# Kernel optimization log

Measured on AMD Instinct MI355X. Metric: run time of the kernel, lower is better.

The kernel has to match this reference:

```python
import jax, jax.numpy as jnp
import numpy as np

L, H, R, N, E = 6, 128, 64, 10000, 160000
SSILU_SCALE = 1.0 / 0.6  # ScaledSiLU
INV_SQRT_3 = 1.0 / np.sqrt(3.0)
INV_SQRT_H = 1.0 / np.sqrt(H)
INV_SQRT_2 = 1.0 / np.sqrt(2.0)


def ssilu(x):
    return jax.nn.silu(x) * SSILU_SCALE


def lnorm(x, w, b):
    m = x.mean(-1, keepdims=True)
    v = jnp.var(x, axis=-1, keepdims=True)
    return (x - m) * jax.lax.rsqrt(v + 1e-5) * w + b


def gated_block(x, v, wv1, wv2, wu1, bu1, wu2, bu2, hout):
    # GatedEquivariantBlock: x [N,Hin], v [N,3,Hin]
    vec1 = jnp.linalg.norm(jnp.einsum('nci,io->nco', v, wv1), axis=-2)  # [N,Hin]
    vec2 = jnp.einsum('nci,io->nco', v, wv2)                            # [N,3,hout]
    h = ssilu(jnp.concatenate([x, vec1], -1) @ wu1 + bu1) @ wu2 + bu2   # [N,2*hout]
    xs, xv = h[..., :hout], h[..., hout:]
    return ssilu(xs), xv[:, None, :] * vec2


def forward_impl(edge_index, x, vec, edge_rbf, edge_vector,
                 ln_w, ln_b, xp1_w, xp1_b, xp2_w, xp2_b, rbf_w, rbf_b,
                 vp_w, xv1_w, xv1_b, xv2_w, xv2_b,
                 we1, be1, we2, be2,
                 g1_v1, g1_v2, g1_u1, g1_u1b, g1_u2, g1_u2b,
                 g2_v1, g2_v2, g2_u1, g2_u1b, g2_u2, g2_u2b):
    src, dst = edge_index[0], edge_index[1]  # message flows src(j) -> dst(i)
    for l in range(L):
        # ---- PaiNNMessage ----
        xh = ssilu(lnorm(x, ln_w[l], ln_b[l]) @ xp1_w[l] + xp1_b[l]) @ xp2_w[l] + xp2_b[l]  # [N,3H]
        rbfh = edge_rbf @ rbf_w[l] + rbf_b[l]                                                # [E,3H]
        m = xh[src] * rbfh                                                                    # gather + elementwise
        mx = m[:, :H]
        m2 = m[:, H:2 * H] * INV_SQRT_3
        m3 = m[:, 2 * H:]
        mvec = (vec[src] * m2[:, None, :] + m3[:, None, :] * edge_vector[:, :, None]) * INV_SQRT_H  # [E,3,H]
        dx = jax.ops.segment_sum(mx, dst, num_segments=N)
        dvec = jax.ops.segment_sum(mvec, dst, num_segments=N)
        x = (x + dx) * INV_SQRT_2
        vec = vec + dvec
        # ---- PaiNNUpdate ----
        vp = jnp.einsum('nci,io->nco', vec, vp_w[l])  # [N,3,2H]
        v1, v2 = vp[..., :H], vp[..., H:]
        vec_dot = (v1 * v2).sum(axis=1) * INV_SQRT_H  # [N,H]
        vnorm = jnp.sqrt((v2 ** 2).sum(axis=-2) + 1e-8)
        h = ssilu(jnp.concatenate([x, vnorm], -1) @ xv1_w[l] + xv1_b[l]) @ xv2_w[l] + xv2_b[l]  # [N,3H]
        xu1, xu2, xu3 = h[:, :H], h[:, H:2 * H], h[:, 2 * H:]
        x = x + (xu1 + xu2 * vec_dot) * INV_SQRT_2
        vec = vec + xu3[:, None, :] * v1
        # ScaleFactor is identity without a scale file
    energy = ssilu(x @ we1 + be1) @ we2 + be2  # [N,1] per-atom energy
    fx, fv = gated_block(x, vec, g1_v1, g1_v2, g1_u1, g1_u1b, g1_u2, g1_u2b, H // 2)
    fx, fv = gated_block(fx, fv, g2_v1, g2_v2, g2_u1, g2_u1b, g2_u2, g2_u2b, 1)
    forces = fv[..., 0]  # [N,3]
    return jnp.concatenate([energy, forces], axis=-1)  # [N,4] packed (energy, fx, fy, fz)


def setup_inputs() -> dict:
    key = jax.random.key(0)
    ks = iter(jax.random.split(key, 64))
    nrm = lambda shape, s=0.05: jax.random.normal(next(ks), shape, jnp.float32) * s
    return dict(
        x=jax.random.normal(next(ks), (N, H), jnp.float32),
        vec=jax.random.normal(next(ks), (N, 3, H), jnp.float32),
        edge_index=jax.random.randint(next(ks), (2, E), 0, N),
        edge_rbf=jax.random.uniform(next(ks), (E, R), jnp.float32),
        edge_vector=jax.random.normal(next(ks), (E, 3), jnp.float32),
        ln_w=jnp.ones((L, H)), ln_b=jnp.zeros((L, H)),
        xp1_w=nrm((L, H, H)), xp1_b=jnp.zeros((L, H)),
        xp2_w=nrm((L, H, 3 * H)), xp2_b=jnp.zeros((L, 3 * H)),
        rbf_w=nrm((L, R, 3 * H)), rbf_b=jnp.zeros((L, 3 * H)),
        vp_w=nrm((L, H, 2 * H)),
        xv1_w=nrm((L, 2 * H, H)), xv1_b=jnp.zeros((L, H)),
        xv2_w=nrm((L, H, 3 * H)), xv2_b=jnp.zeros((L, 3 * H)),
        we1=nrm((H, H // 2)), be1=jnp.zeros((H // 2,)),
        we2=nrm((H // 2, 1)), be2=jnp.zeros((1,)),
        g1_v1=nrm((H, H)), g1_v2=nrm((H, H // 2)),
        g1_u1=nrm((2 * H, H)), g1_u1b=jnp.zeros((H,)),
        g1_u2=nrm((H, H)), g1_u2b=jnp.zeros((H,)),
        g2_v1=nrm((H // 2, H // 2)), g2_v2=nrm((H // 2, 1)),
        g2_u1=nrm((H, H // 2)), g2_u1b=jnp.zeros((H // 2,)),
        g2_u2=nrm((H // 2, 2)), g2_u2b=jnp.zeros((2,)),
    )


def reference(x, vec, edge_index, edge_rbf, edge_vector,
              ln_w, ln_b, xp1_w, xp1_b, xp2_w, xp2_b, rbf_w, rbf_b,
              vp_w, xv1_w, xv1_b, xv2_w, xv2_b,
              we1, be1, we2, be2,
              g1_v1, g1_v2, g1_u1, g1_u1b, g1_u2, g1_u2b,
              g2_v1, g2_v2, g2_u1, g2_u1b, g2_u2, g2_u2b):
    return forward_impl(edge_index, x, vec, edge_rbf, edge_vector,
                        ln_w, ln_b, xp1_w, xp1_b, xp2_w, xp2_b, rbf_w, rbf_b,
                        vp_w, xv1_w, xv1_b, xv2_w, xv2_b,
                        we1, be1, we2, be2,
                        g1_v1, g1_v2, g1_u1, g1_u1b, g1_u2, g1_u2b,
                        g2_v1, g2_v2, g2_u1, g2_u1b, g2_u2, g2_u2b)
```

## Files before the change

kernel.cpp:

```cpp
#include <hip/hip_runtime.h>
#include <hip/hip_bf16.h>

#define NN 10000
#define EE 160000
#define LL 6

#define INV_SQRT_3f  0.57735026919f
#define INV_SQRT_Hf  0.08838834764832f
#define INV_SQRT_2f  0.70710678118655f

typedef _Float16 half8 __attribute__((ext_vector_type(8)));
typedef float f32x4 __attribute__((ext_vector_type(4)));

#define WE1OFF   0
#define WV1OFF   8192
#define WV2OFF   24576
#define WU1OFF   32768
#define WU2OFF   65536
#define G2V1OFF  81920
#define G2U1OFF  86016
#define WFIN_SZ  94208

__device__ __forceinline__ float ssilu_f(float v){
  float s = 1.0f / (1.0f + __expf(-v));
  return v * s * 1.6666666666667f;
}

__global__ __launch_bounds__(256) void k_hist(const int* __restrict__ edst, int* __restrict__ cnt){
  int i = blockIdx.x*256 + threadIdx.x;
  if (i < EE) atomicAdd(&cnt[edst[i]], 1);
}

__global__ __launch_bounds__(1024) void k_scan(const int* __restrict__ cnt,
                                               int* __restrict__ off, int* __restrict__ cur){
  __shared__ int ps[1024];
  int t = threadIdx.x;
  int base = t*10;
  int local[10];
  int s = 0;
  #pragma unroll
  for (int i=0;i<10;i++){
    int c = (base+i < NN) ? cnt[base+i] : 0;
    local[i] = s; s += c;
  }
  ps[t] = s;
  __syncthreads();
  for (int d=1; d<1024; d<<=1){
    int v = (t>=d) ? ps[t-d] : 0;
    __syncthreads();
    ps[t] += v;
    __syncthreads();
  }
  int pre = (t>0) ? ps[t-1] : 0;
  #pragma unroll
  for (int i=0;i<10;i++){
    int idx = base+i;
    if (idx < NN){ int o = pre + local[i]; off[idx]=o; cur[idx]=o; }
  }
  if (t==1023) off[NN] = ps[1023];
}

__global__ __launch_bounds__(256) void k_fill(const int* __restrict__ edst,
                                              int* __restrict__ cur, int* __restrict__ eord){
  int i = blockIdx.x*256 + threadIdx.x;
  if (i < EE){
    int d = edst[i];
    int p = atomicAdd(&cur[d], 1);
    eord[p] = i;
  }
}

__global__ __launch_bounds__(256) void k_sorta(const float* __restrict__ erbf,
                                               const int* __restrict__ eord, _Float16* __restrict__ eA){
  long i = (long)blockIdx.x*256 + threadIdx.x;
  if (i >= (long)EE*64) return;
  int j = i & 7, lane = (i >> 3) & 63, kh = (i >> 9) & 1;
  long tile = i >> 10;
  int e = eord[tile*16 + (lane&15)];
  eA[i] = (_Float16)erbf[(size_t)e*64 + kh*32 + (lane>>4)*8 + j];
}

__global__ __launch_bounds__(256) void k_sorte(const int* __restrict__ esrc, const float* __restrict__ evec,
                                               const int* __restrict__ eord, float4* __restrict__ es4){
  int p = blockIdx.x*256 + threadIdx.x;
  if (p >= EE) return;
  int e = eord[p];
  es4[p] = make_float4(evec[(size_t)e*3], evec[(size_t)e*3+1], evec[(size_t)e*3+2],
                       __int_as_float(esrc[e]));
}

__global__ __launch_bounds__(256) void k_packw(const float* __restrict__ w, _Float16* __restrict__ wf){
  int i = blockIdx.x*256 + threadIdx.x;
  if (i >= LL*24*2*64*8) return;
  int j    = i & 7;
  int lane = (i >> 3) & 63;
  int kh   = (i >> 9) & 1;
  int rest = i >> 10;
  int nb   = rest % 24;
  int l    = rest / 24;
  int k    = 32*kh + 8*(lane>>4) + j;
  int ch   = nb*16 + (lane&15);
  float v = w[((size_t)l*64 + k)*384 + ch];
  if (ch >= 128 && ch < 256) v *= INV_SQRT_3f;
  wf[i] = (_Float16)v;
}

__global__ __launch_bounds__(256) void k_packb(const float* __restrict__ b, float* __restrict__ bsc){
  int i = blockIdx.x*256 + threadIdx.x;
  if (i >= LL*384) return;
  int ch = i % 384;
  float v = b[i];
  if (ch >= 128 && ch < 256) v *= INV_SQRT_3f;
  bsc[i] = v;
}

struct PackTab {
  const float* s[40];
  _Float16* d[40];
  int K[40];
  int NO[40];
};
__global__ __launch_bounds__(256) void k_packall(PackTab tb){
  int e = blockIdx.y;
  int K = tb.K[e], NO = tb.NO[e];
  int tot = K*NO, KS = K >> 5;
  const float* s = tb.s[e];
  _Float16* d = tb.d[e];
  for (int i = blockIdx.x*256 + threadIdx.x; i < tot; i += gridDim.x*256){
    int j = i & 7, lane = (i >> 3) & 63, rest = i >> 9;
    int ks = rest % KS, nb = rest / KS;
    int k = ks*32 + (lane>>4)*8 + j, n = nb*16 + (lane&15);
    d[i] = (_Float16)s[(size_t)k*NO + n];
  }
}

__global__ __launch_bounds__(256) void k_cvt16v(const float* __restrict__ v, _Float16* __restrict__ xv){
  int i = blockIdx.x*256 + threadIdx.x;
  if (i >= NN*384) return;
  int node = i / 384, r = i % 384;
  xv[(size_t)node*768 + 384 + r] = (_Float16)v[i];
}

__global__ __launch_bounds__(256) void k_xhgemm(
    const float* __restrict__ x,
    const float* __restrict__ lnw, const float* __restrict__ lnb,
    const _Float16* __restrict__ wf1, const float* __restrict__ b1,
    const _Float16* __restrict__ wf2, const float* __restrict__ b2,
    _Float16* __restrict__ xv16,
    const _Float16* __restrict__ eA, const _Float16* __restrict__ wf,
    const float* __restrict__ bsc, _Float16* __restrict__ rbfh)
{
  __shared__ _Float16 sA[32][136];
  __shared__ _Float16 sH[32][136];
  int t = threadIdx.x;
  if (blockIdx.x >= 313){
    int ob = (blockIdx.x - 313)*4 + (t >> 6);
    int lane = t & 63;
    int i0 = ob * 64;
    int tg = ob * 4;
    int ml = lane & 15, kg = lane >> 4;
    half8 a0[4], a1[4];
    #pragma unroll
    for (int tt = 0; tt < 4; tt++){
      a0[tt] = *(const half8*)(eA + ((size_t)((tg+tt)*2+0)*64 + lane)*8);
      a1[tt] = *(const half8*)(eA + ((size_t)((tg+tt)*2+1)*64 + lane)*8);
    }
    #pragma unroll 2
    for (int nb = 0; nb < 24; nb++){
      half8 b0 = *(const half8*)(wf + ((size_t)(nb*2+0)*64 + lane)*8);
      half8 b1h = *(const half8*)(wf + ((size_t)(nb*2+1)*64 + lane)*8);
      float bias = bsc[nb*16 + ml];
      #pragma unroll
      for (int tt = 0; tt < 4; tt++){
        f32x4 acc = {bias, bias, bias, bias};
        acc = __builtin_amdgcn_mfma_f32_16x16x32_f16(a0[tt], b0, acc, 0, 0, 0);
        acc = __builtin_amdgcn_mfma_f32_16x16x32_f16(a1[tt], b1h, acc, 0, 0, 0);
        _Float16* orow = rbfh + (size_t)(i0 + tt*16)*384 + nb*16 + ml;
        #pragma unroll
        for (int r = 0; r < 4; r++)
          orow[(size_t)(kg*4 + r)*384] = (_Float16)acc[r];
      }
    }
    return;
  }
  int n0 = blockIdx.x * 32;
  {
    int nd = t >> 3, sb = t & 7;
    int node = n0 + nd;
    float v[16];
    float s = 0.f, ss = 0.f;
    if (node < NN){
      const float* xr = x + (size_t)node*128 + sb*16;
      #pragma unroll
      for (int g = 0; g < 4; g++){
        float4 q = *(const float4*)(xr + g*4);
        v[g*4+0]=q.x; v[g*4+1]=q.y; v[g*4+2]=q.z; v[g*4+3]=q.w;
      }
      #pragma unroll
      for (int u = 0; u < 16; u++){ s += v[u]; ss += v[u]*v[u]; }
    } else {
      #pragma unroll
      for (int u = 0; u < 16; u++) v[u] = 0.f;
    }
    #pragma unroll
    for (int o2 = 4; o2 > 0; o2 >>= 1){
      s  += __shfl_xor(s, o2, 8);
      ss += __shfl_xor(ss, o2, 8);
    }
    float mean = s * (1.0f/128.0f);
    float var  = ss * (1.0f/128.0f) - mean*mean;
    float rstd = rsqrtf(var + 1e-5f);
    #pragma unroll
    for (int u = 0; u < 16; u++){
      int h = sb*16 + u;
      sA[nd][h] = (node < NN) ? (_Float16)((v[u]-mean)*rstd*lnw[h] + lnb[h]) : (_Float16)0.f;
    }
  }
  __syncthreads();
  int lane = t & 63, w = t >> 6, ml = lane & 15, kg = lane >> 4;
  int mt = w >> 1;
  {
    half8 a[4];
    #pragma unroll
    for (int ks = 0; ks < 4; ks++)
      a[ks] = *(const half8*)&sA[mt*16 + ml][ks*32 + kg*8];
    float hout[4][4];
    #pragma unroll
    for (int nb4 = 0; nb4 < 4; nb4++){
      int nb = (w&1)*4 + nb4;
      float bias = b1[nb*16 + ml];
      f32x4 acc = {bias, bias, bias, bias};
      #pragma unroll
      for (int ks = 0; ks < 4; ks++)
        acc = __builtin_amdgcn_mfma_f32_16x16x32_f16(a[ks],
                *(const half8*)(wf1 + ((size_t)(nb*4+ks)*64 + lane)*8), acc, 0,0,0);
      #pragma unroll
      for (int r = 0; r < 4; r++) hout[nb4][r] = ssilu_f(acc[r]);
    }
    #pragma unroll
    for (int nb4 = 0; nb4 < 4; nb4++){
      int nb = (w&1)*4 + nb4;
      #pragma unroll
      for (int r = 0; r < 4; r++)
        sH[mt*16 + kg*4 + r][nb*16 + ml] = (_Float16)hout[nb4][r];
    }
  }
  __syncthreads();
  {
    half8 a[4];
    #pragma unroll
    for (int ks = 0; ks < 4; ks++)
      a[ks] = *(const half8*)&sH[mt*16 + ml][ks*32 + kg*8];
    #pragma unroll 4
    for (int nb12 = 0; nb12 < 12; nb12++){
      int nb = (w&1)*12 + nb12;
      float bias = b2[nb*16 + ml];
      f32x4 acc = {bias, bias, bias, bias};
      #pragma unroll
      for (int ks = 0; ks < 4; ks++)
        acc = __builtin_amdgcn_mfma_f32_16x16x32_f16(a[ks],
                *(const half8*)(wf2 + ((size_t)(nb*4+ks)*64 + lane)*8), acc, 0,0,0);
      #pragma unroll
      for (int r = 0; r < 4; r++){
        int m = mt*16 + kg*4 + r;
        int node = n0 + m;
        if (node < NN) xv16[(size_t)node*768 + nb*16 + ml] = (_Float16)acc[r];
      }
    }
  }
}

__global__ __launch_bounds__(256) void k_edge3(
    const _Float16* __restrict__ rbfh,
    const float4* __restrict__ es4, const int* __restrict__ off,
    const _Float16* __restrict__ xv16,
    _Float16* __restrict__ dx, _Float16* __restrict__ dvec)
{
  int t = threadIdx.x;
  int lane = t & 63;
  int n = blockIdx.x*4 + (t>>6);
  if (n >= NN) return;
  int o0 = off[n], o1 = off[n+1];
  float ax0 = 0.f, ax1 = 0.f;
  float av00=0.f, av01=0.f, av10=0.f, av11=0.f, av20=0.f, av21=0.f;
  #pragma unroll 2
  for (int p = o0; p < o1; p++){
    const _Float16* hr = rbfh + (size_t)p*384;
    float h0 = (float)hr[lane];
    float h1 = (float)hr[64+lane];
    float h2 = (float)hr[128+lane];
    float h3 = (float)hr[192+lane];
    float h4 = (float)hr[256+lane];
    float h5 = (float)hr[320+lane];
    float4 q = es4[p];
    int sN = __float_as_int(q.w);
    const _Float16* xr = xv16 + (size_t)sN*768;
    float m0  = h0 * (float)xr[lane];
    float m1  = h1 * (float)xr[64+lane];
    float m2a = h2 * (float)xr[128+lane];
    float m2b = h3 * (float)xr[192+lane];
    float m3a = h4 * (float)xr[256+lane];
    float m3b = h5 * (float)xr[320+lane];
    ax0 += m0; ax1 += m1;
    const _Float16* vr = xr + 384;
    av00 = fmaf((float)vr[lane],     m2a, av00); av00 = fmaf(m3a, q.x, av00);
    av01 = fmaf((float)vr[64+lane],  m2b, av01); av01 = fmaf(m3b, q.x, av01);
    av10 = fmaf((float)vr[128+lane], m2a, av10); av10 = fmaf(m3a, q.y, av10);
    av11 = fmaf((float)vr[192+lane], m2b, av11); av11 = fmaf(m3b, q.y, av11);
    av20 = fmaf((float)vr[256+lane], m2a, av20); av20 = fmaf(m3a, q.z, av20);
    av21 = fmaf((float)vr[320+lane], m2b, av21); av21 = fmaf(m3b, q.z, av21);
  }
  _Float16* dxr = dx + (size_t)n*128;
  dxr[lane] = (_Float16)ax0; dxr[64+lane] = (_Float16)ax1;
  _Float16* dvr = dvec + (size_t)n*384;
  dvr[lane]     = (_Float16)(av00 * INV_SQRT_Hf);
  dvr[64+lane]  = (_Float16)(av01 * INV_SQRT_Hf);
  dvr[128+lane] = (_Float16)(av10 * INV_SQRT_Hf);
  dvr[192+lane] = (_Float16)(av11 * INV_SQRT_Hf);
  dvr[256+lane] = (_Float16)(av20 * INV_SQRT_Hf);
  dvr[320+lane] = (_Float16)(av21 * INV_SQRT_Hf);
}

__global__ __launch_bounds__(256) void k_node_mfma(
    float* __restrict__ xbuf, float* __restrict__ vbuf,
    const _Float16* __restrict__ dx, const _Float16* __restrict__ dvec,
    const _Float16* __restrict__ wfvp,
    const _Float16* __restrict__ wfxv1, const float* __restrict__ xv1_b,
    const _Float16* __restrict__ wfxv2, const float* __restrict__ xv2_b,
    _Float16* __restrict__ xv16)
{
  __shared__ _Float16 sCat[32][264];
  int t = threadIdx.x;
  int n0 = blockIdx.x * 32;
  int lane = t & 63, w = t >> 6, ml = lane & 15, kg = lane >> 4;
  int mt = w & 1, nbb = (w >> 1) * 4;
  float v1g[3][4][4];
  float vdg[4][4];
  float vn[4][4];
  #pragma unroll
  for (int i=0;i<4;i++){
    #pragma unroll
    for (int r=0;r<4;r++){ vdg[i][r]=0.f; vn[i][r]=0.f; }
  }
  int arow = n0 + mt*16 + ml;
  bool aok = arow < NN;
  #pragma unroll
  for (int cd = 0; cd < 3; cd++){
    half8 a[4];
    #pragma unroll
    for (int ks = 0; ks < 4; ks++){
      if (aok){
        const float* vr = vbuf + (size_t)arow*384 + cd*128 + ks*32 + kg*8;
        const _Float16* dr = dvec + (size_t)arow*384 + cd*128 + ks*32 + kg*8;
        float4 q0 = *(const float4*)(vr);
        float4 q1 = *(const float4*)(vr+4);
        half8 dh = *(const half8*)(dr);
        a[ks][0]=(_Float16)(q0.x+(float)dh[0]); a[ks][1]=(_Float16)(q0.y+(float)dh[1]);
        a[ks][2]=(_Float16)(q0.z+(float)dh[2]); a[ks][3]=(_Float16)(q0.w+(float)dh[3]);
        a[ks][4]=(_Float16)(q1.x+(float)dh[4]); a[ks][5]=(_Float16)(q1.y+(float)dh[5]);
        a[ks][6]=(_Float16)(q1.z+(float)dh[6]); a[ks][7]=(_Float16)(q1.w+(float)dh[7]);
      } else {
        #pragma unroll
        for (int j=0;j<8;j++) a[ks][j] = (_Float16)0.f;
      }
    }
    #pragma unroll
    for (int nb4 = 0; nb4 < 4; nb4++){
      int nb1 = nbb + nb4;
      f32x4 acc1 = {0.f,0.f,0.f,0.f}, acc2 = {0.f,0.f,0.f,0.f};
      #pragma unroll
      for (int ks = 0; ks < 4; ks++){
        acc1 = __builtin_amdgcn_mfma_f32_16x16x32_f16(a[ks],
                 *(const half8*)(wfvp + ((size_t)(nb1*4+ks)*64 + lane)*8), acc1, 0,0,0);
        acc2 = __builtin_amdgcn_mfma_f32_16x16x32_f16(a[ks],
                 *(const half8*)(wfvp + ((size_t)((nb1+8)*4+ks)*64 + lane)*8), acc2, 0,0,0);
      }
      #pragma unroll
      for (int r = 0; r < 4; r++){
        float v1v = acc1[r], v2v = acc2[r];
        vdg[nb4][r] += v1v*v2v;
        vn[nb4][r] += v2v*v2v;
        v1g[cd][nb4][r] = v1v;
      }
    }
  }
  #pragma unroll
  for (int nb4 = 0; nb4 < 4; nb4++){
    #pragma unroll
    for (int r = 0; r < 4; r++){
      int m = mt*16 + kg*4 + r, c = (nbb+nb4)*16 + ml;
      vdg[nb4][r] *= INV_SQRT_Hf;
      sCat[m][128 + c] = (_Float16)sqrtf(vn[nb4][r] + 1e-8f);
    }
  }
  {
    int nd = t >> 3, sb = t & 7;
    int node = n0 + nd;
    if (node < NN){
      const float* xr = xbuf + (size_t)node*128 + sb*16;
      const _Float16* dr = dx + (size_t)node*128 + sb*16;
      half8 da = *(const half8*)(dr);
      half8 db = *(const half8*)(dr+8);
      #pragma unroll
      for (int g = 0; g < 4; g++){
        float4 qa = *(const float4*)(xr + g*4);
        float d0 = (float)((g<2)?da[g*4+0]:db[(g-2)*4+0]);
        float d1 = (float)((g<2)?da[g*4+1]:db[(g-2)*4+1]);
        float d2 = (float)((g<2)?da[g*4+2]:db[(g-2)*4+2]);
        float d3 = (float)((g<2)?da[g*4+3]:db[(g-2)*4+3]);
        sCat[nd][sb*16+g*4+0] = (_Float16)((qa.x+d0)*INV_SQRT_2f);
        sCat[nd][sb*16+g*4+1] = (_Float16)((qa.y+d1)*INV_SQRT_2f);
        sCat[nd][sb*16+g*4+2] = (_Float16)((qa.z+d2)*INV_SQRT_2f);
        sCat[nd][sb*16+g*4+3] = (_Float16)((qa.w+d3)*INV_SQRT_2f);
      }
    } else {
      #pragma unroll
      for (int u = 0; u < 16; u++) sCat[nd][sb*16+u] = (_Float16)0.f;
    }
  }
  __syncthreads();
  float hreg[4][4];
  {
    half8 a[8];
    #pragma unroll
    for (int ks = 0; ks < 8; ks++)
      a[ks] = *(const half8*)&sCat[mt*16 + ml][ks*32 + kg*8];
    #pragma unroll
    for (int nb4 = 0; nb4 < 4; nb4++){
      int nb = (w>>1)*4 + nb4;
      float bias = xv1_b[nb*16 + ml];
      f32x4 acc = {bias, bias, bias, bias};
      #pragma unroll
      for (int ks = 0; ks < 8; ks++)
        acc = __builtin_amdgcn_mfma_f32_16x16x32_f16(a[ks],
                *(const half8*)(wfxv1 + ((size_t)(nb*8+ks)*64 + lane)*8), acc, 0,0,0);
      #pragma unroll
      for (int r = 0; r < 4; r++) hreg[nb4][r] = ssilu_f(acc[r]);
    }
  }
  __syncthreads();
  #pragma unroll
  for (int nb4 = 0; nb4 < 4; nb4++){
    int nb = (w>>1)*4 + nb4;
    #pragma unroll
    for (int r = 0; r < 4; r++)
      sCat[mt*16 + kg*4 + r][nb*16 + ml] = (_Float16)hreg[nb4][r];
  }
  __syncthreads();
  {
    half8 a[4];
    #pragma unroll
    for (int ks = 0; ks < 4; ks++)
      a[ks] = *(const half8*)&sCat[mt*16 + ml][ks*32 + kg*8];
    #pragma unroll 2
    for (int nb4 = 0; nb4 < 4; nb4++){
      int nbu = nbb + nb4;
      float b1v = xv2_b[nbu*16 + ml];
      float b2v = xv2_b[(nbu+8)*16 + ml];
      float b3v = xv2_b[(nbu+16)*16 + ml];
      f32x4 au1 = {b1v,b1v,b1v,b1v};
      f32x4 au2 = {b2v,b2v,b2v,b2v};
      f32x4 au3 = {b3v,b3v,b3v,b3v};
      #pragma unroll
      for (int ks = 0; ks < 4; ks++){
        au1 = __builtin_amdgcn_mfma_f32_16x16x32_f16(a[ks],
                *(const half8*)(wfxv2 + ((size_t)(nbu*4+ks)*64 + lane)*8), au1, 0,0,0);
        au2 = __builtin_amdgcn_mfma_f32_16x16x32_f16(a[ks],
                *(const half8*)(wfxv2 + ((size_t)((nbu+8)*4+ks)*64 + lane)*8), au2, 0,0,0);
        au3 = __builtin_amdgcn_mfma_f32_16x16x32_f16(a[ks],
                *(const half8*)(wfxv2 + ((size_t)((nbu+16)*4+ks)*64 + lane)*8), au3, 0,0,0);
      }
      #pragma unroll
      for (int r = 0; r < 4; r++){
        int m = mt*16 + kg*4 + r;
        int node = n0 + m;
        if (node >= NN) continue;
        int c = nbu*16 + ml;
        float xu1 = au1[r], xu2 = au2[r], xu3 = au3[r];
        float vdv = vdg[nb4][r];
        size_t px = (size_t)node*128 + c;
        float xn = (xbuf[px] + (float)dx[px]) * INV_SQRT_2f;
        xbuf[px] = xn + (xu1 + xu2*vdv) * INV_SQRT_2f;
        #pragma unroll
        for (int cd = 0; cd < 3; cd++){
          float v1v = v1g[cd][nb4][r];
          size_t pv = (size_t)node*384 + cd*128 + c;
          float vo = vbuf[pv] + (float)dvec[pv] + xu3*v1v;
          vbuf[pv] = vo;
          xv16[(size_t)node*768 + 384 + cd*128 + c] = (_Float16)vo;
        }
      }
    }
  }
}

__global__ __launch_bounds__(256) void k_final(
    const float* __restrict__ x, const float* __restrict__ vec,
    const _Float16* __restrict__ wfin,
    const float* __restrict__ be1, const float* __restrict__ we2, const float* __restrict__ be2,
    const float* __restrict__ u1b, const float* __restrict__ u2b,
    const float* __restrict__ g2v2, const float* __restrict__ g2u1b, const float* __restrict__ g2u2,
    const float* __restrict__ g2u2b,
    float* __restrict__ out)
{
  __shared__ _Float16 sCat[32][264];
  __shared__ _Float16 sV2[3][32][72];
  __shared__ _Float16 sH[32][136];
  __shared__ _Float16 sFV[3][32][72];
  __shared__ _Float16 sE1[32][72];
  __shared__ float sR[3][32];
  int t = threadIdx.x;
  int n0 = blockIdx.x * 32;
  int lane = t & 63, w = t >> 6, ml = lane & 15, kg = lane >> 4;
  int mt = w & 1, nh = w >> 1;

  {
    int nd = t >> 3, sb = t & 7;
    int node = n0 + nd;
    if (node < NN){
      const float* xr = x + (size_t)node*128 + sb*16;
      #pragma unroll
      for (int g = 0; g < 4; g++){
        float4 q = *(const float4*)(xr + g*4);
        sCat[nd][sb*16+g*4+0]=(_Float16)q.x; sCat[nd][sb*16+g*4+1]=(_Float16)q.y;
        sCat[nd][sb*16+g*4+2]=(_Float16)q.z; sCat[nd][sb*16+g*4+3]=(_Float16)q.w;
      }
    } else {
      #pragma unroll
      for (int u = 0; u < 16; u++) sCat[nd][sb*16+u] = (_Float16)0.f;
    }
  }
  {
    int arow = n0 + mt*16 + ml;
    bool aok = arow < NN;
    float n1sq[4][4];
    #pragma unroll
    for (int i=0;i<4;i++){
      #pragma unroll
      for (int r=0;r<4;r++) n1sq[i][r]=0.f;
    }
    for (int cd = 0; cd < 3; cd++){
      half8 a[4];
      #pragma unroll
      for (int ks = 0; ks < 4; ks++){
        if (aok){
          const float* vr = vec + (size_t)arow*384 + cd*128 + ks*32 + kg*8;
          float4 q0 = *(const float4*)(vr);
          float4 q1 = *(const float4*)(vr+4);
          a[ks][0]=(_Float16)q0.x; a[ks][1]=(_Float16)q0.y; a[ks][2]=(_Float16)q0.z; a[ks][3]=(_Float16)q0.w;
          a[ks][4]=(_Float16)q1.x; a[ks][5]=(_Float16)q1.y; a[ks][6]=(_Float16)q1.z; a[ks][7]=(_Float16)q1.w;
        } else {
          #pragma unroll
          for (int j=0;j<8;j++) a[ks][j] = (_Float16)0.f;
        }
      }
      #pragma unroll
      for (int nb4 = 0; nb4 < 4; nb4++){
        int nb = nh*4 + nb4;
        f32x4 acc = {0.f,0.f,0.f,0.f};
        #pragma unroll
        for (int ks = 0; ks < 4; ks++)
          acc = __builtin_amdgcn_mfma_f32_16x16x32_f16(a[ks],
                  *(const half8*)(wfin + WV1OFF + ((size_t)(nb*4+ks)*64 + lane)*8), acc, 0,0,0);
        #pragma unroll
        for (int r = 0; r < 4; r++) n1sq[nb4][r] += acc[r]*acc[r];
      }
      #pragma unroll
      for (int q = 0; q < 2; q++){
        int nb = nh*2 + q;
        f32x4 acc = {0.f,0.f,0.f,0.f};
        #pragma unroll
        for (int ks = 0; ks < 4; ks++)
          acc = __builtin_amdgcn_mfma_f32_16x16x32_f16(a[ks],
                  *(const half8*)(wfin + WV2OFF + ((size_t)(nb*4+ks)*64 + lane)*8), acc, 0,0,0);
        #pragma unroll
        for (int r = 0; r < 4; r++)
          sV2[cd][mt*16 + kg*4 + r][nb*16 + ml] = (_Float16)acc[r];
      }
    }
    #pragma unroll
    for (int nb4 = 0; nb4 < 4; nb4++){
      #pragma unroll
      for (int r = 0; r < 4; r++)
        sCat[mt*16 + kg*4 + r][128 + nh*64 + nb4*16 + ml] = (_Float16)sqrtf(n1sq[nb4][r]);
    }
  }
  __syncthreads();
  {
    half8 a[8];
    #pragma unroll
    for (int ks = 0; ks < 8; ks++)
      a[ks] = *(const half8*)&sCat[mt*16 + ml][ks*32 + kg*8];
    #pragma unroll
    for (int q = 0; q < 2; q++){
      int nb = nh*2 + q;
      float bias = be1[nb*16 + ml];
      f32x4 acc = {bias, bias, bias, bias};
      #pragma unroll
      for (int ks = 0; ks < 4; ks++)
        acc = __builtin_amdgcn_mfma_f32_16x16x32_f16(a[ks],
                *(const half8*)(wfin + WE1OFF + ((size_t)(nb*4+ks)*64 + lane)*8), acc, 0,0,0);
      #pragma unroll
      for (int r = 0; r < 4; r++)
        sE1[mt*16 + kg*4 + r][nb*16 + ml] = (_Float16)ssilu_f(acc[r]);
    }
    #pragma unroll
    for (int nb4 = 0; nb4 < 4; nb4++){
      int nb = nh*4 + nb4;
      float bias = u1b[nb*16 + ml];
      f32x4 acc = {bias, bias, bias, bias};
      #pragma unroll
      for (int ks = 0; ks < 8; ks++)
        acc = __builtin_amdgcn_mfma_f32_16x16x32_f16(a[ks],
                *(const half8*)(wfin + WU1OFF + ((size_t)(nb*8+ks)*64 + lane)*8), acc, 0,0,0);
      #pragma unroll
      for (int r = 0; r < 4; r++)
        sH[mt*16 + kg*4 + r][nb*16 + ml] = (_Float16)ssilu_f(acc[r]);
    }
  }
  __syncthreads();
  {
    half8 a[4];
    #pragma unroll
    for (int ks = 0; ks < 4; ks++)
      a[ks] = *(const half8*)&sH[mt*16 + ml][ks*32 + kg*8];
    #pragma unroll
    for (int nb4 = 0; nb4 < 4; nb4++){
      int nb = nh*4 + nb4;
      float bias = u2b[nb*16 + ml];
      f32x4 acc = {bias, bias, bias, bias};
      #pragma unroll
      for (int ks = 0; ks < 4; ks++)
        acc = __builtin_amdgcn_mfma_f32_16x16x32_f16(a[ks],
                *(const half8*)(wfin + WU2OFF + ((size_t)(nb*4+ks)*64 + lane)*8), acc, 0,0,0);
      int c = nb*16 + ml;
      #pragma unroll
      for (int r = 0; r < 4; r++){
        int m = mt*16 + kg*4 + r;
        if (c < 64){
          sCat[m][c] = (_Float16)ssilu_f(acc[r]);
        } else {
          float xv = acc[r];
          #pragma unroll
          for (int cd = 0; cd < 3; cd++)
            sFV[cd][m][c-64] = (_Float16)(xv * (float)sV2[cd][m][c-64]);
        }
      }
    }
    float wev = we2[lane];
    #pragma unroll
    for (int i = 0; i < 8; i++){
      int nd = w*8 + i;
      float v = (float)sE1[nd][lane] * wev;
      #pragma unroll
      for (int o2 = 32; o2 > 0; o2 >>= 1) v += __shfl_xor(v, o2, 64);
      int node = n0 + nd;
      if (lane == 0 && node < NN) out[(size_t)node*4 + 0] = v + be2[0];
    }
  }
  __syncthreads();
  {
    float n1sq[2][4];
    #pragma unroll
    for (int q=0;q<2;q++){
      #pragma unroll
      for (int r=0;r<4;r++) n1sq[q][r]=0.f;
    }
    for (int cd = 0; cd < 3; cd++){
      half8 a[2];
      #pragma unroll
      for (int ks = 0; ks < 2; ks++)
        a[ks] = *(const half8*)&sFV[cd][mt*16 + ml][ks*32 + kg*8];
      #pragma unroll
      for (int q = 0; q < 2; q++){
        int nb = nh*2 + q;
        f32x4 acc = {0.f,0.f,0.f,0.f};
        #pragma unroll
        for (int ks = 0; ks < 2; ks++)
          acc = __builtin_amdgcn_mfma_f32_16x16x32_f16(a[ks],
                  *(const half8*)(wfin + G2V1OFF + ((size_t)(nb*2+ks)*64 + lane)*8), acc, 0,0,0);
        #pragma unroll
        for (int r = 0; r < 4; r++) n1sq[q][r] += acc[r]*acc[r];
      }
    }
    #pragma unroll
    for (int q = 0; q < 2; q++){
      #pragma unroll
      for (int r = 0; r < 4; r++)
        sCat[mt*16 + kg*4 + r][64 + (nh*2+q)*16 + ml] = (_Float16)sqrtf(n1sq[q][r]);
    }
    float g2v = g2v2[lane];
    #pragma unroll
    for (int i = 0; i < 8; i++){
      int nd = w*8 + i;
      #pragma unroll
      for (int cd = 0; cd < 3; cd++){
        float v = (float)sFV[cd][nd][lane] * g2v;
        #pragma unroll
        for (int o2 = 32; o2 > 0; o2 >>= 1) v += __shfl_xor(v, o2, 64);
        if (lane == 0) sR[cd][nd] = v;
      }
    }
  }
  __syncthreads();
  {
    half8 a[4];
    #pragma unroll
    for (int ks = 0; ks < 4; ks++)
      a[ks] = *(const half8*)&sCat[mt*16 + ml][ks*32 + kg*8];
    #pragma unroll
    for (int q = 0; q < 2; q++){
      int nb = nh*2 + q;
      float bias = g2u1b[nb*16 + ml];
      f32x4 acc = {bias, bias, bias, bias};
      #pragma unroll
      for (int ks = 0; ks < 4; ks++)
        acc = __builtin_amdgcn_mfma_f32_16x16x32_f16(a[ks],
                *(const half8*)(wfin + G2U1OFF + ((size_t)(nb*4+ks)*64 + lane)*8), acc, 0,0,0);
      #pragma unroll
      for (int r = 0; r < 4; r++)
        sE1[mt*16 + kg*4 + r][nb*16 + ml] = (_Float16)ssilu_f(acc[r]);
    }
  }
  __syncthreads();
  {
    float g2w = g2u2[lane*2 + 1];
    #pragma unroll
    for (int i = 0; i < 8; i++){
      int nd = w*8 + i;
      float v = (float)sE1[nd][lane] * g2w;
      #pragma unroll
      for (int o2 = 32; o2 > 0; o2 >>= 1) v += __shfl_xor(v, o2, 64);
      int node = n0 + nd;
      if (lane == 0 && node < NN){
        float h21 = v + g2u2b[1];
        out[(size_t)node*4 + 1] = h21 * sR[0][nd];
        out[(size_t)node*4 + 2] = h21 * sR[1][nd];
        out[(size_t)node*4 + 3] = h21 * sR[2][nd];
      }
    }
  }
}

extern "C" void kernel_launch(void* const* d_in, const int* in_sizes, int n_in,
                              void* d_out, int out_size, void* d_ws, size_t ws_size,
                              hipStream_t stream)
{
  const float* x_in   = (const float*)d_in[0];
  const float* vec_in = (const float*)d_in[1];
  const int*   eidx   = (const int*)d_in[2];
  const float* erbf   = (const float*)d_in[3];
  const float* evec   = (const float*)d_in[4];
  const float* ln_w  = (const float*)d_in[5];
  const float* ln_b  = (const float*)d_in[6];
  const float* xp1_w = (const float*)d_in[7];
  const float* xp1_b = (const float*)d_in[8];
  const float* xp2_w = (const float*)d_in[9];
  const float* xp2_b = (const float*)d_in[10];
  const float* rbf_w = (const float*)d_in[11];
  const float* rbf_b = (const float*)d_in[12];
  const float* vp_w  = (const float*)d_in[13];
  const float* xv1_w = (const float*)d_in[14];
  const float* xv1_b = (const float*)d_in[15];
  const float* xv2_w = (const float*)d_in[16];
  const float* xv2_b = (const float*)d_in[17];
  const float* we1 = (const float*)d_in[18];
  const float* be1 = (const float*)d_in[19];
  const float* we2 = (const float*)d_in[20];
  const float* be2 = (const float*)d_in[21];
  const float* g1_v1 = (const float*)d_in[22];
  const float* g1_v2 = (const float*)d_in[23];
  const float* g1_u1 = (const float*)d_in[24];
  const float* g1_u1b = (const float*)d_in[25];
  const float* g1_u2 = (const float*)d_in[26];
  const float* g1_u2b = (const float*)d_in[27];
  const float* g2_v1 = (const float*)d_in[28];
  const float* g2_v2 = (const float*)d_in[29];
  const float* g2_u1 = (const float*)d_in[30];
  const float* g2_u1b = (const float*)d_in[31];
  const float* g2_u2 = (const float*)d_in[32];
  const float* g2_u2b = (const float*)d_in[33];
  float* out = (float*)d_out;

  char* base = (char*)d_ws;
  size_t o = 0;
  auto alloc = [&](size_t bytes) -> char* {
    char* p = base + o;
    o = (o + bytes + 255) & ~(size_t)255;
    return p;
  };
  float* x_cur   = (float*)alloc((size_t)NN*128*4);
  float* vec_cur = (float*)alloc((size_t)NN*384*4);
  _Float16* dx   = (_Float16*)alloc((size_t)NN*128*2);
  _Float16* dvec = (_Float16*)alloc((size_t)NN*384*2);
  _Float16* xv16 = (_Float16*)alloc((size_t)NN*768*2);
  int*   eord    = (int*)alloc((size_t)EE*4);
  int*   off     = (int*)alloc((size_t)(NN+1)*4);
  _Float16* wf   = (_Float16*)alloc((size_t)LL*24576*2);
  float* bsc     = (float*)alloc((size_t)LL*384*4);
  _Float16* wfn  = (_Float16*)alloc((size_t)LL*180224*2);
  _Float16* wfin = (_Float16*)alloc((size_t)WFIN_SZ*2);
  _Float16* eA   = (_Float16*)alloc((size_t)EE*64*2);
  float4* es4    = (float4*)alloc((size_t)EE*16);
  _Float16* rbfh = (_Float16*)alloc((size_t)EE*384*2);
  int* cnt = (int*)dx;
  int* cur = cnt + NN;

  hipMemcpyAsync(x_cur, x_in, sizeof(float)*(size_t)NN*128, hipMemcpyDeviceToDevice, stream);
  hipMemcpyAsync(vec_cur, vec_in, sizeof(float)*(size_t)NN*384, hipMemcpyDeviceToDevice, stream);

  const int* esrc = eidx;
  const int* edst = eidx + EE;

  hipMemsetAsync(cnt, 0, sizeof(int)*NN, stream);
  k_hist<<<(EE+255)/256, 256, 0, stream>>>(edst, cnt);
  k_scan<<<1, 1024, 0, stream>>>(cnt, off, cur);
  k_fill<<<(EE+255)/256, 256, 0, stream>>>(edst, cur, eord);
  k_sorta<<<(EE*64+255)/256, 256, 0, stream>>>(erbf, eord, eA);
  k_sorte<<<(EE+255)/256, 256, 0, stream>>>(esrc, evec, eord, es4);
  k_packw<<<(LL*24576+255)/256, 256, 0, stream>>>(rbf_w, wf);
  k_packb<<<(LL*384+255)/256, 256, 0, stream>>>(rbf_b, bsc);
  k_cvt16v<<<(NN*384+255)/256, 256, 0, stream>>>(vec_in, xv16);

  {
    PackTab tb;
    for (int l = 0; l < LL; l++){
      _Float16* wb = wfn + (size_t)l*180224;
      tb.s[l*5+0] = xp1_w + (size_t)l*128*128; tb.d[l*5+0] = wb;          tb.K[l*5+0]=128; tb.NO[l*5+0]=128;
      tb.s[l*5+1] = xp2_w + (size_t)l*128*384; tb.d[l*5+1] = wb+16384;    tb.K[l*5+1]=128; tb.NO[l*5+1]=384;
      tb.s[l*5+2] = vp_w  + (size_t)l*128*256; tb.d[l*5+2] = wb+65536;    tb.K[l*5+2]=128; tb.NO[l*5+2]=256;
      tb.s[l*5+3] = xv1_w + (size_t)l*256*128; tb.d[l*5+3] = wb+98304;    tb.K[l*5+3]=256; tb.NO[l*5+3]=128;
      tb.s[l*5+4] = xv2_w + (size_t)l*128*384; tb.d[l*5+4] = wb+131072;   tb.K[l*5+4]=128; tb.NO[l*5+4]=384;
    }
    tb.s[30] = we1;   tb.d[30] = wfin + WE1OFF;  tb.K[30]=128; tb.NO[30]=64;
    tb.s[31] = g1_v1; tb.d[31] = wfin + WV1OFF;  tb.K[31]=128; tb.NO[31]=128;
    tb.s[32] = g1_v2; tb.d[32] = wfin + WV2OFF;  tb.K[32]=128; tb.NO[32]=64;
    tb.s[33] = g1_u1; tb.d[33] = wfin + WU1OFF;  tb.K[33]=256; tb.NO[33]=128;
    tb.s[34] = g1_u2; tb.d[34] = wfin + WU2OFF;  tb.K[34]=128; tb.NO[34]=128;
    tb.s[35] = g2_v1; tb.d[35] = wfin + G2V1OFF; tb.K[35]=64;  tb.NO[35]=64;
    tb.s[36] = g2_u1; tb.d[36] = wfin + G2U1OFF; tb.K[36]=128; tb.NO[36]=64;
    k_packall<<<dim3(24, 37), 256, 0, stream>>>(tb);
  }

  for (int l = 0; l < LL; l++){
    _Float16* wb = wfn + (size_t)l*180224;
    k_xhgemm<<<938, 256, 0, stream>>>(x_cur, ln_w + l*128, ln_b + l*128,
        wb, xp1_b + l*128, wb+16384, xp2_b + l*384, xv16,
        eA, wf + (size_t)l*24576, bsc + (size_t)l*384, rbfh);
    k_edge3<<<NN/4, 256, 0, stream>>>(rbfh, es4, off, xv16, dx, dvec);
    k_node_mfma<<<(NN+31)/32, 256, 0, stream>>>(x_cur, vec_cur, dx, dvec,
        wb+65536, wb+98304, xv1_b + l*128, wb+131072, xv2_b + l*384, xv16);
  }
  k_final<<<(NN+31)/32, 256, 0, stream>>>(x_cur, vec_cur, wfin,
      be1, we2, be2, g1_u1b, g1_u2b, g2_v2, g2_u1b, g2_u2, g2_u2b, out);
}
```

Before: 905.9 us.

## Keep vector state only in fp16 buffer and prefetch next edge descriptor

Drops the fp32 vec_cur state and makes the fp16 copy inside xv16 the only stored vector state. The node update kernel and the final kernel now read and write it directly, which removes fp32 vector reads and writes plus one device-to-device copy. The edge kernel also loads the next edge's packed src/vector descriptor one iteration ahead to hide its latency. The risk is that the residual vector state now accumulates in fp16 across all six layers, which may hurt accuracy.

```diff
diff --git a/kernel.cpp b/kernel.cpp
--- a/kernel.cpp
+++ b/kernel.cpp
@@ -283,8 +283,10 @@
   int o0 = off[n], o1 = off[n+1];
   float ax0 = 0.f, ax1 = 0.f;
   float av00=0.f, av01=0.f, av10=0.f, av11=0.f, av20=0.f, av21=0.f;
+  float4 q = (o0 < o1) ? es4[o0] : make_float4(0.f,0.f,0.f,0.f);
   #pragma unroll 2
   for (int p = o0; p < o1; p++){
+    float4 qn = (p+1 < o1) ? es4[p+1] : q;
     const _Float16* hr = rbfh + (size_t)p*384;
     float h0 = (float)hr[lane];
     float h1 = (float)hr[64+lane];
@@ -292,7 +294,6 @@
     float h3 = (float)hr[192+lane];
     float h4 = (float)hr[256+lane];
     float h5 = (float)hr[320+lane];
-    float4 q = es4[p];
     int sN = __float_as_int(q.w);
     const _Float16* xr = xv16 + (size_t)sN*768;
     float m0  = h0 * (float)xr[lane];
@@ -309,6 +310,7 @@
     av11 = fmaf((float)vr[192+lane], m2b, av11); av11 = fmaf(m3b, q.y, av11);
     av20 = fmaf((float)vr[256+lane], m2a, av20); av20 = fmaf(m3a, q.z, av20);
     av21 = fmaf((float)vr[320+lane], m2b, av21); av21 = fmaf(m3b, q.z, av21);
+    q = qn;
   }
   _Float16* dxr = dx + (size_t)n*128;
   dxr[lane] = (_Float16)ax0; dxr[64+lane] = (_Float16)ax1;
@@ -322,7 +324,7 @@
 }
 
 __global__ __launch_bounds__(256) void k_node_mfma(
-    float* __restrict__ xbuf, float* __restrict__ vbuf,
+    float* __restrict__ xbuf,
     const _Float16* __restrict__ dx, const _Float16* __restrict__ dvec,
     const _Float16* __restrict__ wfvp,
     const _Float16* __restrict__ wfxv1, const float* __restrict__ xv1_b,
@@ -350,15 +352,13 @@
     #pragma unroll
     for (int ks = 0; ks < 4; ks++){
       if (aok){
-        const float* vr = vbuf + (size_t)arow*384 + cd*128 + ks*32 + kg*8;
+        const _Float16* vr16 = xv16 + (size_t)arow*768 + 384 + cd*128 + ks*32 + kg*8;
         const _Float16* dr = dvec + (size_t)arow*384 + cd*128 + ks*32 + kg*8;
-        float4 q0 = *(const float4*)(vr);
-        float4 q1 = *(const float4*)(vr+4);
+        half8 vh = *(const half8*)(vr16);
         half8 dh = *(const half8*)(dr);
-        a[ks][0]=(_Float16)(q0.x+(float)dh[0]); a[ks][1]=(_Float16)(q0.y+(float)dh[1]);
-        a[ks][2]=(_Float16)(q0.z+(float)dh[2]); a[ks][3]=(_Float16)(q0.w+(float)dh[3]);
-        a[ks][4]=(_Float16)(q1.x+(float)dh[4]); a[ks][5]=(_Float16)(q1.y+(float)dh[5]);
-        a[ks][6]=(_Float16)(q1.z+(float)dh[6]); a[ks][7]=(_Float16)(q1.w+(float)dh[7]);
+        #pragma unroll
+        for (int j = 0; j < 8; j++)
+          a[ks][j] = (_Float16)((float)vh[j] + (float)dh[j]);
       } else {
         #pragma unroll
         for (int j=0;j<8;j++) a[ks][j] = (_Float16)0.f;
@@ -484,10 +484,10 @@
         #pragma unroll
         for (int cd = 0; cd < 3; cd++){
           float v1v = v1g[cd][nb4][r];
-          size_t pv = (size_t)node*384 + cd*128 + c;
-          float vo = vbuf[pv] + (float)dvec[pv] + xu3*v1v;
-          vbuf[pv] = vo;
-          xv16[(size_t)node*768 + 384 + cd*128 + c] = (_Float16)vo;
+          size_t pv16 = (size_t)node*768 + 384 + cd*128 + c;
+          size_t pdv  = (size_t)node*384 + cd*128 + c;
+          float vo = (float)xv16[pv16] + (float)dvec[pdv] + xu3*v1v;
+          xv16[pv16] = (_Float16)vo;
         }
       }
     }
@@ -495,7 +495,7 @@
 }
 
 __global__ __launch_bounds__(256) void k_final(
-    const float* __restrict__ x, const float* __restrict__ vec,
+    const float* __restrict__ x, const _Float16* __restrict__ xv16,
     const _Float16* __restrict__ wfin,
     const float* __restrict__ be1, const float* __restrict__ we2, const float* __restrict__ be2,
     const float* __restrict__ u1b, const float* __restrict__ u2b,
@@ -544,11 +544,7 @@
       #pragma unroll
       for (int ks = 0; ks < 4; ks++){
         if (aok){
-          const float* vr = vec + (size_t)arow*384 + cd*128 + ks*32 + kg*8;
-          float4 q0 = *(const float4*)(vr);
-          float4 q1 = *(const float4*)(vr+4);
-          a[ks][0]=(_Float16)q0.x; a[ks][1]=(_Float16)q0.y; a[ks][2]=(_Float16)q0.z; a[ks][3]=(_Float16)q0.w;
-          a[ks][4]=(_Float16)q1.x; a[ks][5]=(_Float16)q1.y; a[ks][6]=(_Float16)q1.z; a[ks][7]=(_Float16)q1.w;
+          a[ks] = *(const half8*)(xv16 + (size_t)arow*768 + 384 + cd*128 + ks*32 + kg*8);
         } else {
           #pragma unroll
           for (int j=0;j<8;j++) a[ks][j] = (_Float16)0.f;
@@ -790,7 +786,6 @@
     return p;
   };
   float* x_cur   = (float*)alloc((size_t)NN*128*4);
-  float* vec_cur = (float*)alloc((size_t)NN*384*4);
   _Float16* dx   = (_Float16*)alloc((size_t)NN*128*2);
   _Float16* dvec = (_Float16*)alloc((size_t)NN*384*2);
   _Float16* xv16 = (_Float16*)alloc((size_t)NN*768*2);
@@ -803,11 +798,10 @@
   _Float16* eA   = (_Float16*)alloc((size_t)EE*64*2);
   float4* es4    = (float4*)alloc((size_t)EE*16);
   _Float16* rbfh = (_Float16*)alloc((size_t)EE*384*2);
-  int* cnt = (int*)dx;
+  int* cnt = (int*)dvec;
   int* cur = cnt + NN;
 
   hipMemcpyAsync(x_cur, x_in, sizeof(float)*(size_t)NN*128, hipMemcpyDeviceToDevice, stream);
-  hipMemcpyAsync(vec_cur, vec_in, sizeof(float)*(size_t)NN*384, hipMemcpyDeviceToDevice, stream);
 
   const int* esrc = eidx;
   const int* edst = eidx + EE;
@@ -848,9 +842,9 @@
         wb, xp1_b + l*128, wb+16384, xp2_b + l*384, xv16,
         eA, wf + (size_t)l*24576, bsc + (size_t)l*384, rbfh);
     k_edge3<<<NN/4, 256, 0, stream>>>(rbfh, es4, off, xv16, dx, dvec);
-    k_node_mfma<<<(NN+31)/32, 256, 0, stream>>>(x_cur, vec_cur, dx, dvec,
+    k_node_mfma<<<(NN+31)/32, 256, 0, stream>>>(x_cur, dx, dvec,
         wb+65536, wb+98304, xv1_b + l*128, wb+131072, xv2_b + l*384, xv16);
   }
-  k_final<<<(NN+31)/32, 256, 0, stream>>>(x_cur, vec_cur, wfin,
+  k_final<<<(NN+31)/32, 256, 0, stream>>>(x_cur, xv16, wfin,
       be1, we2, be2, g1_u1b, g1_u2b, g2_v2, g2_u1b, g2_u2, g2_u2b, out);
 }
```

Measured after the change: 953.9 us. 1.05x slower.
